# Performance work log

Measured on AMD Instinct MI355X. Metric: run time of the kernel, lower is better.

## Reference

```python
import jax, jax.numpy as jnp
import numpy as np

N = 1024          # nodes per atom and per input graph / barycenter
K = 8             # num_atoms
OT_LAYERS = 3     # proximal-point outer iterations inside fgwd
SINKHORN_LAYERS = 3
GWB_LAYERS = 2    # barycenter alternating-optimization iterations
PROX_BETA = 0.1   # proximal / entropic regularization strength
EPS = 1e-16


def fgwd(Gs, ps, Gb, pb):
    """Gromov-Wasserstein distance via proximal point + Sinkhorn.
    Gs:(ns,ns), ps:(ns,1), Gb:(nb,nb), pb:(nb,1). Returns (d, T) with T:(ns,nb).
    Square-loss GW cost: c(T) = f1(Gs) ps 1^T + 1 (f2(Gb) pb)^T - 2 Gs T Gb^T."""
    ns, nb = Gs.shape[0], Gb.shape[0]
    cost_st = ((Gs * Gs) @ ps) + ((Gb * Gb) @ pb).T  # (ns,1)+(1,nb) -> (ns,nb)
    T0 = ps @ pb.T  # independent-coupling init

    def ot_step(T, _):
        cost = cost_st - 2.0 * (Gs @ T @ Gb.T)
        kernel = jnp.exp(-cost / PROX_BETA) * T  # proximal-point kernel

        def sink(carry, _):
            a, b = carry
            b = pb / (kernel.T @ a + EPS)
            a = ps / (kernel @ b + EPS)
            return (a, b), None

        (a, b), _ = jax.lax.scan(sink, (ps, pb), None, length=SINKHORN_LAYERS)
        return (a * kernel) * b.T, None

    T, _ = jax.lax.scan(ot_step, T0, None, length=OT_LAYERS)
    cost = cost_st - 2.0 * (Gs @ T @ Gb.T)
    d = jnp.sum(cost * T)
    return d, T


def setup_inputs() -> dict:
    key = jax.random.key(0)
    k1, k2, k3 = jax.random.split(key, 3)
    Gm = jax.random.uniform(k1, (N, N), jnp.float32)          # input graph (sigmoid-range adjacency)
    pm = jnp.ones((N, 1), jnp.float32) / N                    # uniform node distribution
    atoms_presig = jax.random.normal(k2, (K, N, N), jnp.float32)  # pre-sigmoid atom params
    probs = jnp.ones((K, N, 1), jnp.float32) / N              # uniform atom distributions
    weights = jax.nn.softmax(jax.random.normal(k3, (K,), jnp.float32))  # output_weights
    return {"Gm": Gm, "pm": pm, "atoms_presig": atoms_presig, "probs": probs,
            "weights": weights}


def reference(Gm, pm, atoms_presig, probs, weights):
    Gk = jax.nn.sigmoid(atoms_presig)              # output_atoms: (K,N,N)
    G_bary, pb = Gm, pm                            # init_mode=0 -> barycenter init from input M
    fgwd_v = jax.vmap(fgwd, in_axes=(0, 0, None, None))
    denom = pb @ pb.T                              # pb pb^T normalizer
    for _ in range(GWB_LAYERS):
        _, trans = fgwd_v(Gk, probs, G_bary, pb)   # trans: (K,N,N)
        # comp_fgwb: sum_k w_k * T_k^T G_k T_k / (pb pb^T)
        GT = jnp.einsum('knm,kmj->knj', Gk, trans)
        G_bary = jnp.einsum('k,kni,knj->ij', weights, trans, GT) / denom
    d_fgw, _ = fgwd(Gm, pm, G_bary, pb)
    return d_fgw, G_bary
```

## Files before the change

kernel.cpp:

```cpp
#include <hip/hip_runtime.h>
#include <math.h>

#define N_   1024
#define K_   8
#define OTL  3
#define SKL  3
#define GWBL 2
#define INVB 10.0f
#define EPSV 1e-16f
#define INVN (1.0f / 1024.0f)
#define NN   ((size_t)N_ * N_)

typedef __attribute__((ext_vector_type(8))) short short8;
typedef __attribute__((ext_vector_type(4))) float f32x4;
typedef unsigned short bfu;

__device__ __forceinline__ float b2f(bfu u) {
    unsigned x = ((unsigned)u) << 16;
    return __builtin_bit_cast(float, x);
}
__device__ __forceinline__ bfu f2b(float f) {
    unsigned u = __builtin_bit_cast(unsigned, f);
    unsigned r = u + 0x7fffu + ((u >> 16) & 1u);
    return (bfu)(r >> 16);
}

template<int EPI>
__global__ __launch_bounds__(256, 2)
void bgemm_k(const bfu* __restrict__ A, const bfu* __restrict__ B,
             void* __restrict__ Cp, size_t sA, size_t sB, size_t sC,
             const float* __restrict__ rv, const float* __restrict__ cv,
             const float* __restrict__ wts, float* __restrict__ rs) {
    __shared__ bfu As[128 * 32];
    __shared__ bfu Bs[128 * 32];

    const int z  = blockIdx.x;
    const int bm = blockIdx.y * 128, bn = blockIdx.z * 128;
    const int tid = threadIdx.x;
    const int lane = tid & 63, wv = tid >> 6;
    const int wr = wv >> 1, wc = wv & 1;

    if (EPI == 0) {
        if (rs && blockIdx.y == 0 && blockIdx.z == 0) {
            float4 zf = {0.f, 0.f, 0.f, 0.f};
            *(float4*)&rs[z * N_ + tid * 4] = zf;
        }
    }

    const bfu* Az = A + (size_t)z * sA;
    const bfu* Bz = B + (size_t)z * sB;

    const int sr = tid >> 2;
    const int sk = (tid & 3) * 8;
    const int fr = lane & 15;
    const int ks = (lane >> 4) * 8;

    f32x4 acc[4][4];
    #pragma unroll
    for (int i = 0; i < 4; i++)
        #pragma unroll
        for (int j = 0; j < 4; j++) acc[i][j] = (f32x4)0.f;

    for (int k0 = 0; k0 < N_; k0 += 32) {
        __syncthreads();
        #pragma unroll
        for (int h = 0; h < 2; ++h) {
            const int row = sr + h * 64;
            const bfu* ga = Az + (size_t)(bm + row) * N_ + k0 + sk;
            const bfu* gb = Bz + (size_t)(bn + row) * N_ + k0 + sk;
            __builtin_amdgcn_global_load_lds(
                (const __attribute__((address_space(1))) unsigned int*)ga,
                (__attribute__((address_space(3))) unsigned int*)&As[row * 32 + sk],
                16, 0, 0);
            __builtin_amdgcn_global_load_lds(
                (const __attribute__((address_space(1))) unsigned int*)gb,
                (__attribute__((address_space(3))) unsigned int*)&Bs[row * 32 + sk],
                16, 0, 0);
        }
        __syncthreads();

        short8 af[4], bf[4];
        #pragma unroll
        for (int mi = 0; mi < 4; ++mi)
            af[mi] = *(const short8*)&As[(wr * 64 + mi * 16 + fr) * 32 + ks];
        #pragma unroll
        for (int ni = 0; ni < 4; ++ni)
            bf[ni] = *(const short8*)&Bs[(wc * 64 + ni * 16 + fr) * 32 + ks];
        #pragma unroll
        for (int mi = 0; mi < 4; ++mi)
            #pragma unroll
            for (int ni = 0; ni < 4; ++ni)
                acc[mi][ni] = __builtin_amdgcn_mfma_f32_16x16x32_bf16(
                    af[mi], bf[ni], acc[mi][ni], 0, 0, 0);
    }

    const int r0 = bm + wr * 64, c0 = bn + wc * 64;
    const int rq = (lane >> 4) * 4;

    if (EPI == 1) {
        float* Cz = (float*)Cp + (size_t)z * sC;
        const float w = wts[z];
        #pragma unroll
        for (int mi = 0; mi < 4; ++mi)
            #pragma unroll
            for (int ni = 0; ni < 4; ++ni)
                #pragma unroll
                for (int q = 0; q < 4; ++q)
                    Cz[(size_t)(r0 + mi * 16 + rq + q) * N_ + c0 + ni * 16 + fr]
                        = w * acc[mi][ni][q];
    } else if (EPI == 0) {
        bfu* Cz = (bfu*)Cp + (size_t)z * sC;
        #pragma unroll
        for (int mi = 0; mi < 4; ++mi)
            #pragma unroll
            for (int ni = 0; ni < 4; ++ni)
                #pragma unroll
                for (int q = 0; q < 4; ++q)
                    Cz[(size_t)(r0 + mi * 16 + rq + q) * N_ + c0 + ni * 16 + fr]
                        = f2b(acc[mi][ni][q]);
    } else {
        bfu* Cz = (bfu*)Cp + (size_t)z * sC;
        const float* rvz = rv + z * N_;
        float rsum[4][4];
        #pragma unroll
        for (int mi = 0; mi < 4; ++mi)
            #pragma unroll
            for (int q = 0; q < 4; ++q) rsum[mi][q] = 0.f;
        #pragma unroll
        for (int mi = 0; mi < 4; ++mi)
            #pragma unroll
            for (int ni = 0; ni < 4; ++ni)
                #pragma unroll
                for (int q = 0; q < 4; ++q) {
                    const int row = r0 + mi * 16 + rq + q;
                    const int col = c0 + ni * 16 + fr;
                    const float cost = rvz[col] + cv[row] - 2.f * acc[mi][ni][q];
                    const float t = b2f(Cz[(size_t)row * N_ + col]);
                    const bfu tn = f2b(expf(-cost * INVB) * t);
                    Cz[(size_t)row * N_ + col] = tn;
                    rsum[mi][q] += b2f(tn);
                }
        #pragma unroll
        for (int mi = 0; mi < 4; ++mi)
            #pragma unroll
            for (int q = 0; q < 4; ++q) {
                float v = rsum[mi][q];
                v += __shfl_xor(v, 1);
                v += __shfl_xor(v, 2);
                v += __shfl_xor(v, 4);
                v += __shfl_xor(v, 8);
                if (fr == 0)
                    atomicAdd(&rs[z * N_ + r0 + mi * 16 + rq + q], v);
            }
    }
}

__global__ __launch_bounds__(256, 2)
void gemm_splitk_k(const bfu* __restrict__ A, const bfu* __restrict__ B,
                   float* __restrict__ P) {
    __shared__ bfu As[128 * 32];
    __shared__ bfu Bs[128 * 32];
    const int bn = blockIdx.x * 128;
    const int bm = blockIdx.y * 128;
    const int kbase = blockIdx.z * 256;
    const int tid = threadIdx.x;
    const int lane = tid & 63, wv = tid >> 6;
    const int wr = wv >> 1, wc = wv & 1;
    const int sr = tid >> 2, sk = (tid & 3) * 8;
    const int fr = lane & 15, ks = (lane >> 4) * 8;

    f32x4 acc[4][4];
    #pragma unroll
    for (int i = 0; i < 4; i++)
        #pragma unroll
        for (int j = 0; j < 4; j++) acc[i][j] = (f32x4)0.f;

    for (int k0 = kbase; k0 < kbase + 256; k0 += 32) {
        __syncthreads();
        #pragma unroll
        for (int h = 0; h < 2; ++h) {
            const int row = sr + h * 64;
            __builtin_amdgcn_global_load_lds(
                (const __attribute__((address_space(1))) unsigned int*)
                    (A + (size_t)(bm + row) * N_ + k0 + sk),
                (__attribute__((address_space(3))) unsigned int*)&As[row * 32 + sk],
                16, 0, 0);
            __builtin_amdgcn_global_load_lds(
                (const __attribute__((address_space(1))) unsigned int*)
                    (B + (size_t)(bn + row) * N_ + k0 + sk),
                (__attribute__((address_space(3))) unsigned int*)&Bs[row * 32 + sk],
                16, 0, 0);
        }
        __syncthreads();
        short8 af[4], bf[4];
        #pragma unroll
        for (int mi = 0; mi < 4; ++mi)
            af[mi] = *(const short8*)&As[(wr * 64 + mi * 16 + fr) * 32 + ks];
        #pragma unroll
        for (int ni = 0; ni < 4; ++ni)
            bf[ni] = *(const short8*)&Bs[(wc * 64 + ni * 16 + fr) * 32 + ks];
        #pragma unroll
        for (int mi = 0; mi < 4; ++mi)
            #pragma unroll
            for (int ni = 0; ni < 4; ++ni)
                acc[mi][ni] = __builtin_amdgcn_mfma_f32_16x16x32_bf16(
                    af[mi], bf[ni], acc[mi][ni], 0, 0, 0);
    }

    float* Pz = P + (size_t)blockIdx.z * NN;
    const int r0 = bm + wr * 64, c0 = bn + wc * 64;
    const int rq = (lane >> 4) * 4;
    #pragma unroll
    for (int mi = 0; mi < 4; ++mi)
        #pragma unroll
        for (int ni = 0; ni < 4; ++ni)
            #pragma unroll
            for (int q = 0; q < 4; ++q)
                Pz[(size_t)(r0 + mi * 16 + rq + q) * N_ + c0 + ni * 16 + fr]
                    = acc[mi][ni][q];
}

template<int EPI>
__global__ void comb_k(const float* __restrict__ P, bfu* __restrict__ Tt,
                       const float* __restrict__ rv, const float* __restrict__ cv,
                       float* __restrict__ dout, const float* __restrict__ pb,
                       float* __restrict__ bv) {
    const int tid = threadIdx.x;
    if (EPI == 0) {
        if (dout && blockIdx.x == 0 && tid == 0) *dout = 0.f;
    }
    __shared__ float red[4];
    float bs = 0.f;
    #pragma unroll
    for (int rep = 0; rep < 2; ++rep) {
        const int row = blockIdx.x + rep * 512;
        const size_t idx = (size_t)row * N_ + tid * 4;
        float4 s = *(const float4*)(P + idx);
        #pragma unroll
        for (int sl = 1; sl < 4; ++sl) {
            float4 v = *(const float4*)(P + (size_t)sl * NN + idx);
            s.x += v.x; s.y += v.y; s.z += v.z; s.w += v.w;
        }
        if (EPI == 0) {
            bfu o[4];
            o[0] = f2b(s.x); o[1] = f2b(s.y); o[2] = f2b(s.z); o[3] = f2b(s.w);
            *(ulong1*)&Tt[idx] = *(ulong1*)o;
        } else {
            const int c = tid * 4;
            const float cvr = cv[row];
            const float4 rvc = *(const float4*)(rv + c);
            bfu t[4];
            *(ulong1*)t = *(const ulong1*)&Tt[idx];
            if (EPI == 2) {
                t[0] = f2b(expf(-(rvc.x + cvr - 2.f * s.x) * INVB) * b2f(t[0]));
                t[1] = f2b(expf(-(rvc.y + cvr - 2.f * s.y) * INVB) * b2f(t[1]));
                t[2] = f2b(expf(-(rvc.z + cvr - 2.f * s.z) * INVB) * b2f(t[2]));
                t[3] = f2b(expf(-(rvc.w + cvr - 2.f * s.w) * INVB) * b2f(t[3]));
                *(ulong1*)&Tt[idx] = *(ulong1*)t;
                float rsm = b2f(t[0]) + b2f(t[1]) + b2f(t[2]) + b2f(t[3]);
                #pragma unroll
                for (int off = 32; off; off >>= 1) rsm += __shfl_down(rsm, off);
                if ((tid & 63) == 0) red[tid >> 6] = rsm;
                __syncthreads();
                if (tid == 0)
                    bv[row] = pb[row] /
                        ((red[0] + red[1] + red[2] + red[3]) * INVN + EPSV);
                __syncthreads();
            } else {
                bs += (rvc.x + cvr - 2.f * s.x) * b2f(t[0]);
                bs += (rvc.y + cvr - 2.f * s.y) * b2f(t[1]);
                bs += (rvc.z + cvr - 2.f * s.z) * b2f(t[2]);
                bs += (rvc.w + cvr - 2.f * s.w) * b2f(t[3]);
            }
        }
    }
    if (EPI == 3) {
        #pragma unroll
        for (int off = 32; off; off >>= 1) bs += __shfl_down(bs, off);
        if ((tid & 63) == 0) red[tid >> 6] = bs;
        __syncthreads();
        if (tid == 0) atomicAdd(dout, red[0] + red[1] + red[2] + red[3]);
    }
}

__global__ __launch_bounds__(256)
void prox1_k(bfu* __restrict__ Tt, const float* __restrict__ c2,
             const float* __restrict__ u, const float* __restrict__ d2,
             const float* __restrict__ w, const float* __restrict__ ps,
             const float* __restrict__ pb, float* __restrict__ bv,
             int zs, int nb) {
    const int b = blockIdx.x;
    const int z  = (nb == 8) ? (b & 7) : 0;
    const int rp = (nb == 8) ? (b >> 3) : b;
    const int tid = threadIdx.x;
    const int half = tid >> 7;
    const int j = rp * 2 + half;
    const int i0 = (tid & 127) * 8;
    const float d2j = d2[j], wj = w[j], pbj = pb[j];
    const float* c2z = c2 + z * zs + i0;
    const float* uz  = u  + z * zs + i0;
    const float* psz = ps + z * zs + i0;
    bfu o[8];
    float s = 0.f;
    #pragma unroll
    for (int t = 0; t < 8; ++t) {
        const float cost = c2z[t] + d2j - 2.f * uz[t] * wj;
        o[t] = f2b(expf(-cost * INVB) * psz[t] * pbj);
        s += b2f(o[t]);
    }
    *(short8*)&Tt[((size_t)z << 20) + ((size_t)j << 10) + i0] = *(short8*)o;
    #pragma unroll
    for (int off = 32; off; off >>= 1) s += __shfl_down(s, off);
    __shared__ float red[4];
    if ((tid & 63) == 0) red[tid >> 6] = s;
    __syncthreads();
    if ((tid & 127) == 0)
        bv[z * N_ + j] = pbj / ((red[half * 2] + red[half * 2 + 1]) * INVN + EPSV);
}


__global__ void sinkb_k(const bfu* __restrict__ Tt, const float* __restrict__ a0,
                        const float* __restrict__ pb, float* __restrict__ bv) {
    int z, jb;
    if (gridDim.y == 8) { z = blockIdx.x & 7; jb = (blockIdx.x >> 3) + (blockIdx.y << 5); }
    else                { z = 0;              jb = blockIdx.x; }
    const int wv = threadIdx.x >> 6, lane = threadIdx.x & 63;
    const int j = jb * 4 + wv;
    const bfu* Tr = Tt + (size_t)z * NN + (size_t)j * N_;
    const float* az = a0 + z * N_;
    float s = 0.f;
    for (int c = lane * 8; c < N_; c += 512) {
        bfu t[8];
        *(short8*)t = *(const short8*)&Tr[c];
        #pragma unroll
        for (int q = 0; q < 8; ++q) s += b2f(t[q]) * az[c + q];
    }
    #pragma unroll
    for (int off = 32; off; off >>= 1) s += __shfl_down(s, off);
    if (lane == 0) bv[z * N_ + j] = pb[j] / (s + EPSV);
}

template<int NB, int RS, int TUPD>
__global__ __launch_bounds__(1024)
void sinka_k(bfu* __restrict__ Tt, const float* __restrict__ bvin,
             const float* __restrict__ rs, const float* __restrict__ ps, int pstr,
             float* __restrict__ av) {
    constexpr int CPB = (NB == 8) ? 32 : 16;
    constexpr int RG  = 1024 / CPB;
    constexpr int RPG = N_ / RG;
    int z, cb;
    if (NB == 8) { z = blockIdx.x & 7; cb = blockIdx.x >> 3; }
    else         { z = 0;              cb = blockIdx.x; }
    const int tid = threadIdx.x;
    const int cl = tid % CPB, rg = tid / CPB;
    const int i = cb * CPB + cl;
    bfu* Tz = Tt + (size_t)z * NN;

    __shared__ float bvs[1024];
    __shared__ float red[1024];
    if (RS) bvs[tid] = INVN / (rs[z * N_ + tid] * INVN + EPSV);
    else    bvs[tid] = bvin[z * N_ + tid];
    __syncthreads();

    float s = 0.f;
    const int j0 = rg * RPG;
    #pragma unroll 8
    for (int j = j0; j < j0 + RPG; ++j)
        s += b2f(Tz[(size_t)j * N_ + i]) * bvs[j];
    red[tid] = s;
    __syncthreads();
    #pragma unroll
    for (int h = RG / 2; h > 0; h >>= 1) {
        if (rg < h) red[rg * CPB + cl] += red[(rg + h) * CPB + cl];
        __syncthreads();
    }
    const float avi = ps[z * pstr + i] / (red[cl] + EPSV);
    if (!TUPD) {
        if (rg == 0) av[z * N_ + i] = avi;
    } else {
        for (int j = j0; j < j0 + RPG; ++j) {
            const size_t o = (size_t)j * N_ + i;
            Tz[o] = f2b(b2f(Tz[o]) * avi * bvs[j]);
        }
    }
}


template<int SIG>
__global__ void prep_k(const float* __restrict__ X, bfu* __restrict__ Y,
                       float* __restrict__ y2, float* __restrict__ y1) {
    const int z = blockIdx.y;
    const int wv = threadIdx.x >> 6, lane = threadIdx.x & 63;
    const int r = blockIdx.x * 4 + wv;
    const float* Xr = X + (size_t)z * NN + (size_t)r * N_;
    bfu* Yr = Y + (size_t)z * NN + (size_t)r * N_;
    float s2 = 0.f, s1 = 0.f;
    for (int c = lane * 4; c < N_; c += 256) {
        float4 v = *(const float4*)(Xr + c);
        if (SIG) {
            v.x = 1.f / (1.f + expf(-v.x));
            v.y = 1.f / (1.f + expf(-v.y));
            v.z = 1.f / (1.f + expf(-v.z));
            v.w = 1.f / (1.f + expf(-v.w));
        }
        bfu o[4];
        o[0] = f2b(v.x); o[1] = f2b(v.y); o[2] = f2b(v.z); o[3] = f2b(v.w);
        *(ulong1*)&Yr[c] = *(ulong1*)o;
        s2 += v.x * v.x + v.y * v.y + v.z * v.z + v.w * v.w;
        s1 += v.x + v.y + v.z + v.w;
    }
    #pragma unroll
    for (int off = 32; off; off >>= 1) {
        s2 += __shfl_down(s2, off);
        s1 += __shfl_down(s1, off);
    }
    if (lane == 0) {
        y2[z * N_ + r] = s2 * INVN;
        y1[z * N_ + r] = s1 * INVN;
    }
}

__global__ void reduce8_k(const float* __restrict__ part, bfu* __restrict__ Gbt,
                          float* __restrict__ d2, float* __restrict__ w,
                          float* __restrict__ out1) {
    const int tid = threadIdx.x;
    __shared__ float wred[2][8];
    #pragma unroll
    for (int rep = 0; rep < 2; ++rep) {
        const int row = blockIdx.x + rep * 512;
        const size_t idx = (size_t)row * N_ + tid * 4;
        float4 s = *(const float4*)(part + idx);
        #pragma unroll
        for (int sl = 1; sl < K_; ++sl) {
            float4 v = *(const float4*)(part + (size_t)sl * NN + idx);
            s.x += v.x; s.y += v.y; s.z += v.z; s.w += v.w;
        }
        const float sc = 1048576.f;
        s.x *= sc; s.y *= sc; s.z *= sc; s.w *= sc;
        bfu o[4];
        o[0] = f2b(s.x); o[1] = f2b(s.y); o[2] = f2b(s.z); o[3] = f2b(s.w);
        *(ulong1*)&Gbt[idx] = *(ulong1*)o;
        if (out1) {
            out1[idx + 0] = s.x; out1[idx + 1] = s.y;
            out1[idx + 2] = s.z; out1[idx + 3] = s.w;
        }
        float r2 = s.x * s.x + s.y * s.y + s.z * s.z + s.w * s.w;
        float r1 = s.x + s.y + s.z + s.w;
        #pragma unroll
        for (int off = 32; off; off >>= 1) {
            r2 += __shfl_down(r2, off);
            r1 += __shfl_down(r1, off);
        }
        if ((tid & 63) == 0) {
            wred[0][(tid >> 6) * 2]     = r2;
            wred[0][(tid >> 6) * 2 + 1] = r1;
        }
        __syncthreads();
        if (tid == 0) {
            d2[row] = (wred[0][0] + wred[0][2] + wred[0][4] + wred[0][6]) * INVN;
            w[row]  = (wred[0][1] + wred[0][3] + wred[0][5] + wred[0][7]) * INVN;
        }
        __syncthreads();
    }
}


template<int NB, int RS1>
static inline void sink_tail(bfu* Tt, const float* ps, int pstr, const float* pm,
                             float* avec, float* bvec, float* rs, hipStream_t stream) {
    const dim3 ga((NB == 8) ? 256 : 64);
    const dim3 gb(256, NB);
    const dim3 blk(256);
    sinka_k<NB, RS1, 0><<<ga, dim3(1024), 0, stream>>>(Tt, bvec, rs, ps, pstr, avec);
    sinkb_k<<<gb, blk, 0, stream>>>(Tt, avec, pm, bvec);
    sinka_k<NB, 0, 0><<<ga, dim3(1024), 0, stream>>>(Tt, bvec, rs, ps, pstr, avec);
    sinkb_k<<<gb, blk, 0, stream>>>(Tt, avec, pm, bvec);
    sinka_k<NB, 0, 1><<<ga, dim3(1024), 0, stream>>>(Tt, bvec, rs, ps, pstr, avec);
}

extern "C" void kernel_launch(void* const* d_in, const int* in_sizes, int n_in,
                              void* d_out, int out_size, void* d_ws, size_t ws_size,
                              hipStream_t stream) {
    const float* Gm    = (const float*)d_in[0];
    const float* pm    = (const float*)d_in[1];
    const float* atoms = (const float*)d_in[2];
    const float* probs = (const float*)d_in[3];
    const float* wts   = (const float*)d_in[4];
    float* out = (float*)d_out;

    char* base = (char*)d_ws;
    bfu*   Gkt  = (bfu*)base;                    base += K_ * NN * 2;
    bfu*   Tt   = (bfu*)base;                    base += K_ * NN * 2;
    bfu*   M    = (bfu*)base;                    base += K_ * NN * 2;
    float* part = (float*)base;                  base += K_ * NN * 4;
    bfu*   Gbt  = (bfu*)base;                    base += NN * 2;
    bfu*   Gmt  = (bfu*)base;                    base += NN * 2;
    float* Gk2ps = (float*)base;                 base += K_ * N_ * 4;
    float* Gku   = (float*)base;                 base += K_ * N_ * 4;
    float* Gm2pm = (float*)base;                 base += N_ * 4;
    float* Gmu   = (float*)base;                 base += N_ * 4;
    float* Gb2pb = (float*)base;                 base += N_ * 4;
    float* Gbw   = (float*)base;                 base += N_ * 4;
    float* avec  = (float*)base;                 base += K_ * N_ * 4;
    float* bvec  = (float*)base;                 base += K_ * N_ * 4;
    float* rs    = (float*)base;                 base += K_ * N_ * 4;

    const dim3 blk(256);
    const dim3 g8(8, 8, 8);
    const dim3 gsk(8, 8, 4);

    prep_k<1><<<dim3(256, K_), blk, 0, stream>>>(atoms, Gkt, Gk2ps, Gku);
    prep_k<0><<<dim3(256, 1), blk, 0, stream>>>(Gm, Gmt, Gm2pm, Gmu);

    for (int it = 0; it < GWBL; ++it) {
        const bfu*   GbtU = it ? Gbt : Gmt;
        const float* d2U  = it ? Gb2pb : Gm2pm;
        const float* wU   = it ? Gbw : Gmu;

        prox1_k<<<512 * K_, blk, 0, stream>>>(Tt, Gk2ps, Gku, d2U, wU,
                                              probs, pm, bvec, N_, K_);
        sink_tail<K_, 0>(Tt, probs, N_, pm, avec, bvec, rs, stream);
        for (int ot = 1; ot < OTL; ++ot) {
            bgemm_k<0><<<g8, blk, 0, stream>>>(Gkt, Tt, M, NN, NN, NN,
                nullptr, nullptr, nullptr, rs);
            bgemm_k<2><<<g8, blk, 0, stream>>>(GbtU, M, Tt, 0, NN, NN,
                Gk2ps, d2U, nullptr, rs);
            sink_tail<K_, 1>(Tt, probs, N_, pm, avec, bvec, rs, stream);
        }
        bgemm_k<0><<<g8, blk, 0, stream>>>(Tt, Gkt, M, NN, NN, NN,
            nullptr, nullptr, nullptr, nullptr);
        bgemm_k<1><<<g8, blk, 0, stream>>>(Tt, M, part, NN, NN, NN,
            nullptr, nullptr, wts, nullptr);
        reduce8_k<<<512, blk, 0, stream>>>(part, Gbt, Gb2pb, Gbw,
                                           (it == GWBL - 1) ? out + 1 : nullptr);
    }

    prox1_k<<<512, blk, 0, stream>>>(Tt, Gm2pm, Gmu, Gb2pb, Gbw, pm, pm, bvec, 0, 1);
    sink_tail<1, 0>(Tt, pm, 0, pm, avec, bvec, rs, stream);
    for (int ot = 1; ot < OTL; ++ot) {
        gemm_splitk_k<<<gsk, blk, 0, stream>>>(Gmt, Tt, part);
        comb_k<0><<<512, blk, 0, stream>>>(part, M, nullptr, nullptr,
                                           nullptr, nullptr, nullptr);
        gemm_splitk_k<<<gsk, blk, 0, stream>>>(Gbt, M, part);
        comb_k<2><<<512, blk, 0, stream>>>(part, Tt, Gm2pm, Gb2pb,
                                           nullptr, pm, bvec);
        sink_tail<1, 0>(Tt, pm, 0, pm, avec, bvec, rs, stream);
    }
    gemm_splitk_k<<<gsk, blk, 0, stream>>>(Gmt, Tt, part);
    comb_k<0><<<512, blk, 0, stream>>>(part, M, nullptr, nullptr,
                                       out , nullptr, nullptr);
    gemm_splitk_k<<<gsk, blk, 0, stream>>>(Gbt, M, part);
    comb_k<3><<<512, blk, 0, stream>>>(part, Tt, Gm2pm, Gb2pb, out, nullptr, nullptr);
}
```

Before: 684.3 us.

## Fuse Sinkhorn iterations into cooperative kernel and replace split-K GEMM with fused-epilogue tiles

The separate Sinkhorn row/column kernels become one cooperative kernel. It loops over all Sinkhorn iterations and uses grid-wide syncs in place of several kernel launches. The final single-graph GW stage now uses a 64x64-tile GEMM with the cost/exp, row-sum or distance epilogue fused in. This removes the split-K partial buffers and the separate combine kernels. The costs are grid.sync overhead, occupancy limits from requiring all 256 blocks of 1024 threads to be co-resident, and a smaller GEMM tile with less data reuse.

```diff
diff --git a/kernel.cpp b/kernel.cpp
--- a/kernel.cpp
+++ b/kernel.cpp
@@ -1,5 +1,8 @@
 #include <hip/hip_runtime.h>
+#include <hip/hip_cooperative_groups.h>
 #include <math.h>
+
+namespace cg = cooperative_groups;
 
 #define N_   1024
 #define K_   8
@@ -155,131 +158,132 @@
     }
 }
 
+template<int EPI>
 __global__ __launch_bounds__(256, 2)
-void gemm_splitk_k(const bfu* __restrict__ A, const bfu* __restrict__ B,
-                   float* __restrict__ P) {
-    __shared__ bfu As[128 * 32];
-    __shared__ bfu Bs[128 * 32];
-    const int bn = blockIdx.x * 128;
-    const int bm = blockIdx.y * 128;
-    const int kbase = blockIdx.z * 256;
+void gemm64_k(const bfu* __restrict__ A, const bfu* __restrict__ B,
+              void* __restrict__ Cp,
+              const float* __restrict__ rv, const float* __restrict__ cv,
+              float* __restrict__ rs, float* __restrict__ dout) {
+    __shared__ bfu As[64 * 32];
+    __shared__ bfu Bs[64 * 32];
+    const int bn = blockIdx.x * 64;
+    const int bm = blockIdx.y * 64;
     const int tid = threadIdx.x;
     const int lane = tid & 63, wv = tid >> 6;
     const int wr = wv >> 1, wc = wv & 1;
     const int sr = tid >> 2, sk = (tid & 3) * 8;
     const int fr = lane & 15, ks = (lane >> 4) * 8;
 
-    f32x4 acc[4][4];
+    if (EPI == 0) {
+        if (blockIdx.x == 0 && blockIdx.y == 0) {
+            if (rs) {
+                float4 zf = {0.f, 0.f, 0.f, 0.f};
+                *(float4*)&rs[tid * 4] = zf;
+            }
+            if (dout && tid == 0) *dout = 0.f;
+        }
+    }
+
+    f32x4 acc[2][2];
     #pragma unroll
-    for (int i = 0; i < 4; i++)
-        #pragma unroll
-        for (int j = 0; j < 4; j++) acc[i][j] = (f32x4)0.f;
-
-    for (int k0 = kbase; k0 < kbase + 256; k0 += 32) {
-        __syncthreads();
-        #pragma unroll
-        for (int h = 0; h < 2; ++h) {
-            const int row = sr + h * 64;
-            __builtin_amdgcn_global_load_lds(
-                (const __attribute__((address_space(1))) unsigned int*)
-                    (A + (size_t)(bm + row) * N_ + k0 + sk),
-                (__attribute__((address_space(3))) unsigned int*)&As[row * 32 + sk],
-                16, 0, 0);
-            __builtin_amdgcn_global_load_lds(
-                (const __attribute__((address_space(1))) unsigned int*)
-                    (B + (size_t)(bn + row) * N_ + k0 + sk),
-                (__attribute__((address_space(3))) unsigned int*)&Bs[row * 32 + sk],
-                16, 0, 0);
-        }
-        __syncthreads();
-        short8 af[4], bf[4];
-        #pragma unroll
-        for (int mi = 0; mi < 4; ++mi)
-            af[mi] = *(const short8*)&As[(wr * 64 + mi * 16 + fr) * 32 + ks];
-        #pragma unroll
-        for (int ni = 0; ni < 4; ++ni)
-            bf[ni] = *(const short8*)&Bs[(wc * 64 + ni * 16 + fr) * 32 + ks];
-        #pragma unroll
-        for (int mi = 0; mi < 4; ++mi)
-            #pragma unroll
-            for (int ni = 0; ni < 4; ++ni)
+    for (int i = 0; i < 2; i++)
+        #pragma unroll
+        for (int j = 0; j < 2; j++) acc[i][j] = (f32x4)0.f;
+
+    for (int k0 = 0; k0 < N_; k0 += 32) {
+        __syncthreads();
+        __builtin_amdgcn_global_load_lds(
+            (const __attribute__((address_space(1))) unsigned int*)
+                (A + (size_t)(bm + sr) * N_ + k0 + sk),
+            (__attribute__((address_space(3))) unsigned int*)&As[sr * 32 + sk],
+            16, 0, 0);
+        __builtin_amdgcn_global_load_lds(
+            (const __attribute__((address_space(1))) unsigned int*)
+                (B + (size_t)(bn + sr) * N_ + k0 + sk),
+            (__attribute__((address_space(3))) unsigned int*)&Bs[sr * 32 + sk],
+            16, 0, 0);
+        __syncthreads();
+        short8 af[2], bf[2];
+        #pragma unroll
+        for (int mi = 0; mi < 2; ++mi)
+            af[mi] = *(const short8*)&As[(wr * 32 + mi * 16 + fr) * 32 + ks];
+        #pragma unroll
+        for (int ni = 0; ni < 2; ++ni)
+            bf[ni] = *(const short8*)&Bs[(wc * 32 + ni * 16 + fr) * 32 + ks];
+        #pragma unroll
+        for (int mi = 0; mi < 2; ++mi)
+            #pragma unroll
+            for (int ni = 0; ni < 2; ++ni)
                 acc[mi][ni] = __builtin_amdgcn_mfma_f32_16x16x32_bf16(
                     af[mi], bf[ni], acc[mi][ni], 0, 0, 0);
     }
 
-    float* Pz = P + (size_t)blockIdx.z * NN;
-    const int r0 = bm + wr * 64, c0 = bn + wc * 64;
+    const int r0 = bm + wr * 32, c0 = bn + wc * 32;
     const int rq = (lane >> 4) * 4;
-    #pragma unroll
-    for (int mi = 0; mi < 4; ++mi)
-        #pragma unroll
-        for (int ni = 0; ni < 4; ++ni)
-            #pragma unroll
-            for (int q = 0; q < 4; ++q)
-                Pz[(size_t)(r0 + mi * 16 + rq + q) * N_ + c0 + ni * 16 + fr]
-                    = acc[mi][ni][q];
-}
-
-template<int EPI>
-__global__ void comb_k(const float* __restrict__ P, bfu* __restrict__ Tt,
-                       const float* __restrict__ rv, const float* __restrict__ cv,
-                       float* __restrict__ dout, const float* __restrict__ pb,
-                       float* __restrict__ bv) {
-    const int tid = threadIdx.x;
+
     if (EPI == 0) {
-        if (dout && blockIdx.x == 0 && tid == 0) *dout = 0.f;
-    }
-    __shared__ float red[4];
-    float bs = 0.f;
-    #pragma unroll
-    for (int rep = 0; rep < 2; ++rep) {
-        const int row = blockIdx.x + rep * 512;
-        const size_t idx = (size_t)row * N_ + tid * 4;
-        float4 s = *(const float4*)(P + idx);
-        #pragma unroll
-        for (int sl = 1; sl < 4; ++sl) {
-            float4 v = *(const float4*)(P + (size_t)sl * NN + idx);
-            s.x += v.x; s.y += v.y; s.z += v.z; s.w += v.w;
-        }
-        if (EPI == 0) {
-            bfu o[4];
-            o[0] = f2b(s.x); o[1] = f2b(s.y); o[2] = f2b(s.z); o[3] = f2b(s.w);
-            *(ulong1*)&Tt[idx] = *(ulong1*)o;
-        } else {
-            const int c = tid * 4;
-            const float cvr = cv[row];
-            const float4 rvc = *(const float4*)(rv + c);
-            bfu t[4];
-            *(ulong1*)t = *(const ulong1*)&Tt[idx];
-            if (EPI == 2) {
-                t[0] = f2b(expf(-(rvc.x + cvr - 2.f * s.x) * INVB) * b2f(t[0]));
-                t[1] = f2b(expf(-(rvc.y + cvr - 2.f * s.y) * INVB) * b2f(t[1]));
-                t[2] = f2b(expf(-(rvc.z + cvr - 2.f * s.z) * INVB) * b2f(t[2]));
-                t[3] = f2b(expf(-(rvc.w + cvr - 2.f * s.w) * INVB) * b2f(t[3]));
-                *(ulong1*)&Tt[idx] = *(ulong1*)t;
-                float rsm = b2f(t[0]) + b2f(t[1]) + b2f(t[2]) + b2f(t[3]);
-                #pragma unroll
-                for (int off = 32; off; off >>= 1) rsm += __shfl_down(rsm, off);
-                if ((tid & 63) == 0) red[tid >> 6] = rsm;
-                __syncthreads();
-                if (tid == 0)
-                    bv[row] = pb[row] /
-                        ((red[0] + red[1] + red[2] + red[3]) * INVN + EPSV);
-                __syncthreads();
-            } else {
-                bs += (rvc.x + cvr - 2.f * s.x) * b2f(t[0]);
-                bs += (rvc.y + cvr - 2.f * s.y) * b2f(t[1]);
-                bs += (rvc.z + cvr - 2.f * s.z) * b2f(t[2]);
-                bs += (rvc.w + cvr - 2.f * s.w) * b2f(t[3]);
+        bfu* C = (bfu*)Cp;
+        #pragma unroll
+        for (int mi = 0; mi < 2; ++mi)
+            #pragma unroll
+            for (int ni = 0; ni < 2; ++ni)
+                #pragma unroll
+                for (int q = 0; q < 4; ++q)
+                    C[(size_t)(r0 + mi * 16 + rq + q) * N_ + c0 + ni * 16 + fr]
+                        = f2b(acc[mi][ni][q]);
+    } else if (EPI == 2) {
+        bfu* C = (bfu*)Cp;
+        float rsum[2][4];
+        #pragma unroll
+        for (int mi = 0; mi < 2; ++mi)
+            #pragma unroll
+            for (int q = 0; q < 4; ++q) rsum[mi][q] = 0.f;
+        #pragma unroll
+        for (int mi = 0; mi < 2; ++mi)
+            #pragma unroll
+            for (int ni = 0; ni < 2; ++ni)
+                #pragma unroll
+                for (int q = 0; q < 4; ++q) {
+                    const int row = r0 + mi * 16 + rq + q;
+                    const int col = c0 + ni * 16 + fr;
+                    const float cost = rv[col] + cv[row] - 2.f * acc[mi][ni][q];
+                    const float t = b2f(C[(size_t)row * N_ + col]);
+                    const bfu tn = f2b(expf(-cost * INVB) * t);
+                    C[(size_t)row * N_ + col] = tn;
+                    rsum[mi][q] += b2f(tn);
+                }
+        #pragma unroll
+        for (int mi = 0; mi < 2; ++mi)
+            #pragma unroll
+            for (int q = 0; q < 4; ++q) {
+                float v = rsum[mi][q];
+                v += __shfl_xor(v, 1);
+                v += __shfl_xor(v, 2);
+                v += __shfl_xor(v, 4);
+                v += __shfl_xor(v, 8);
+                if (fr == 0)
+                    atomicAdd(&rs[r0 + mi * 16 + rq + q], v);
             }
-        }
-    }
-    if (EPI == 3) {
+    } else {
+        const bfu* C = (const bfu*)Cp;
+        float bs = 0.f;
+        #pragma unroll
+        for (int mi = 0; mi < 2; ++mi)
+            #pragma unroll
+            for (int ni = 0; ni < 2; ++ni)
+                #pragma unroll
+                for (int q = 0; q < 4; ++q) {
+                    const int row = r0 + mi * 16 + rq + q;
+                    const int col = c0 + ni * 16 + fr;
+                    bs += (rv[col] + cv[row] - 2.f * acc[mi][ni][q]) *
+                          b2f(C[(size_t)row * N_ + col]);
+                }
         #pragma unroll
         for (int off = 32; off; off >>= 1) bs += __shfl_down(bs, off);
-        if ((tid & 63) == 0) red[tid >> 6] = bs;
-        __syncthreads();
-        if (tid == 0) atomicAdd(dout, red[0] + red[1] + red[2] + red[3]);
+        __shared__ float wred[4];
+        if (lane == 0) wred[wv] = bs;
+        __syncthreads();
+        if (tid == 0) atomicAdd(dout, wred[0] + wred[1] + wred[2] + wred[3]);
     }
 }
 
@@ -318,69 +322,79 @@
         bv[z * N_ + j] = pbj / ((red[half * 2] + red[half * 2 + 1]) * INVN + EPSV);
 }
 
-
-__global__ void sinkb_k(const bfu* __restrict__ Tt, const float* __restrict__ a0,
-                        const float* __restrict__ pb, float* __restrict__ bv) {
-    int z, jb;
-    if (gridDim.y == 8) { z = blockIdx.x & 7; jb = (blockIdx.x >> 3) + (blockIdx.y << 5); }
-    else                { z = 0;              jb = blockIdx.x; }
-    const int wv = threadIdx.x >> 6, lane = threadIdx.x & 63;
-    const int j = jb * 4 + wv;
-    const bfu* Tr = Tt + (size_t)z * NN + (size_t)j * N_;
-    const float* az = a0 + z * N_;
-    float s = 0.f;
-    for (int c = lane * 8; c < N_; c += 512) {
-        bfu t[8];
-        *(short8*)t = *(const short8*)&Tr[c];
-        #pragma unroll
-        for (int q = 0; q < 8; ++q) s += b2f(t[q]) * az[c + q];
-    }
-    #pragma unroll
-    for (int off = 32; off; off >>= 1) s += __shfl_down(s, off);
-    if (lane == 0) bv[z * N_ + j] = pb[j] / (s + EPSV);
-}
-
-template<int NB, int RS, int TUPD>
-__global__ __launch_bounds__(1024)
-void sinka_k(bfu* __restrict__ Tt, const float* __restrict__ bvin,
-             const float* __restrict__ rs, const float* __restrict__ ps, int pstr,
-             float* __restrict__ av) {
+template<int NB, int RS1>
+__global__ __launch_bounds__(1024, 1)
+void sink_fused_k(bfu* __restrict__ Tt, const float* __restrict__ rs,
+                  const float* __restrict__ bv1,
+                  const float* __restrict__ ps, int pstr,
+                  const float* __restrict__ pb,
+                  float* __restrict__ av, float* __restrict__ bv) {
+    cg::grid_group grid = cg::this_grid();
     constexpr int CPB = (NB == 8) ? 32 : 16;
     constexpr int RG  = 1024 / CPB;
     constexpr int RPG = N_ / RG;
+    constexpr int RPB = (NB == 8) ? 32 : 16;
+    constexpr int RPW = RPB / 16;
+
+    const int blk = blockIdx.x;
     int z, cb;
-    if (NB == 8) { z = blockIdx.x & 7; cb = blockIdx.x >> 3; }
-    else         { z = 0;              cb = blockIdx.x; }
+    if (NB == 8) { z = blk & 7; cb = blk >> 3; }
+    else         { z = 0;       cb = blk; }
     const int tid = threadIdx.x;
     const int cl = tid % CPB, rg = tid / CPB;
     const int i = cb * CPB + cl;
+    const int wv = tid >> 6, lane = tid & 63;
+    const int rb0 = cb * RPB;
+    const int zN = z * N_;
     bfu* Tz = Tt + (size_t)z * NN;
+    const float psv = ps[z * pstr + i];
+    const int j0 = rg * RPG;
 
     __shared__ float bvs[1024];
     __shared__ float red[1024];
-    if (RS) bvs[tid] = INVN / (rs[z * N_ + tid] * INVN + EPSV);
-    else    bvs[tid] = bvin[z * N_ + tid];
-    __syncthreads();
-
-    float s = 0.f;
-    const int j0 = rg * RPG;
-    #pragma unroll 8
-    for (int j = j0; j < j0 + RPG; ++j)
-        s += b2f(Tz[(size_t)j * N_ + i]) * bvs[j];
-    red[tid] = s;
-    __syncthreads();
-    #pragma unroll
-    for (int h = RG / 2; h > 0; h >>= 1) {
-        if (rg < h) red[rg * CPB + cl] += red[(rg + h) * CPB + cl];
-        __syncthreads();
-    }
-    const float avi = ps[z * pstr + i] / (red[cl] + EPSV);
-    if (!TUPD) {
-        if (rg == 0) av[z * N_ + i] = avi;
-    } else {
-        for (int j = j0; j < j0 + RPG; ++j) {
-            const size_t o = (size_t)j * N_ + i;
-            Tz[o] = f2b(b2f(Tz[o]) * avi * bvs[j]);
+
+    for (int it = 0; it < SKL; ++it) {
+        if (it == 0) bvs[tid] = RS1 ? (INVN / (rs[zN + tid] * INVN + EPSV))
+                                    : bv1[zN + tid];
+        else         bvs[tid] = bv[zN + tid];
+        __syncthreads();
+        float s = 0.f;
+        #pragma unroll 8
+        for (int j = j0; j < j0 + RPG; ++j)
+            s += b2f(Tz[(size_t)j * N_ + i]) * bvs[j];
+        red[tid] = s;
+        __syncthreads();
+        #pragma unroll
+        for (int h = RG / 2; h > 0; h >>= 1) {
+            if (rg < h) red[rg * CPB + cl] += red[(rg + h) * CPB + cl];
+            __syncthreads();
+        }
+        const float avi = psv / (red[cl] + EPSV);
+        if (it == SKL - 1) {
+            for (int j = j0; j < j0 + RPG; ++j) {
+                const size_t o = (size_t)j * N_ + i;
+                Tz[o] = f2b(b2f(Tz[o]) * avi * bvs[j]);
+            }
+        } else {
+            if (rg == 0) av[zN + i] = avi;
+            grid.sync();
+            #pragma unroll
+            for (int rr = 0; rr < RPW; ++rr) {
+                const int j = rb0 + wv * RPW + rr;
+                const bfu* Tr = Tz + (size_t)j * N_;
+                const float* az = av + zN;
+                float sb = 0.f;
+                for (int c = lane * 8; c < N_; c += 512) {
+                    bfu t[8];
+                    *(short8*)t = *(const short8*)&Tr[c];
+                    #pragma unroll
+                    for (int q = 0; q < 8; ++q) sb += b2f(t[q]) * az[c + q];
+                }
+                #pragma unroll
+                for (int off = 32; off; off >>= 1) sb += __shfl_down(sb, off);
+                if (lane == 0) bv[zN + j] = pb[j] / (sb + EPSV);
+            }
+            grid.sync();
         }
     }
 }
@@ -424,7 +438,7 @@
                           float* __restrict__ d2, float* __restrict__ w,
                           float* __restrict__ out1) {
     const int tid = threadIdx.x;
-    __shared__ float wred[2][8];
+    __shared__ float wred[8];
     #pragma unroll
     for (int rep = 0; rep < 2; ++rep) {
         const int row = blockIdx.x + rep * 512;
@@ -452,31 +466,18 @@
             r1 += __shfl_down(r1, off);
         }
         if ((tid & 63) == 0) {
-            wred[0][(tid >> 6) * 2]     = r2;
-            wred[0][(tid >> 6) * 2 + 1] = r1;
+            wred[(tid >> 6) * 2]     = r2;
+            wred[(tid >> 6) * 2 + 1] = r1;
         }
         __syncthreads();
         if (tid == 0) {
-            d2[row] = (wred[0][0] + wred[0][2] + wred[0][4] + wred[0][6]) * INVN;
-            w[row]  = (wred[0][1] + wred[0][3] + wred[0][5] + wred[0][7]) * INVN;
-        }
-        __syncthreads();
-    }
-}
-
-
-template<int NB, int RS1>
-static inline void sink_tail(bfu* Tt, const float* ps, int pstr, const float* pm,
-                             float* avec, float* bvec, float* rs, hipStream_t stream) {
-    const dim3 ga((NB == 8) ? 256 : 64);
-    const dim3 gb(256, NB);
-    const dim3 blk(256);
-    sinka_k<NB, RS1, 0><<<ga, dim3(1024), 0, stream>>>(Tt, bvec, rs, ps, pstr, avec);
-    sinkb_k<<<gb, blk, 0, stream>>>(Tt, avec, pm, bvec);
-    sinka_k<NB, 0, 0><<<ga, dim3(1024), 0, stream>>>(Tt, bvec, rs, ps, pstr, avec);
-    sinkb_k<<<gb, blk, 0, stream>>>(Tt, avec, pm, bvec);
-    sinka_k<NB, 0, 1><<<ga, dim3(1024), 0, stream>>>(Tt, bvec, rs, ps, pstr, avec);
-}
+            d2[row] = (wred[0] + wred[2] + wred[4] + wred[6]) * INVN;
+            w[row]  = (wred[1] + wred[3] + wred[5] + wred[7]) * INVN;
+        }
+        __syncthreads();
+    }
+}
+
 
 extern "C" void kernel_launch(void* const* d_in, const int* in_sizes, int n_in,
                               void* d_out, int out_size, void* d_ws, size_t ws_size,
@@ -507,7 +508,17 @@
 
     const dim3 blk(256);
     const dim3 g8(8, 8, 8);
-    const dim3 gsk(8, 8, 4);
+    const dim3 g64(16, 16);
+
+    bfu* TtP = Tt;
+    float* rsP = rs;
+    float* bvecP = bvec;
+    const float* probsP = probs;
+    const float* pmP = pm;
+    float* avP = avec;
+    int pstrN = N_, pstr0 = 0;
+    void* argsB[] = { &TtP, &rsP, &bvecP, &probsP, &pstrN, &pmP, &avP, &bvecP };
+    void* args1[] = { &TtP, &rsP, &bvecP, &pmP,    &pstr0, &pmP, &avP, &bvecP };
 
     prep_k<1><<<dim3(256, K_), blk, 0, stream>>>(atoms, Gkt, Gk2ps, Gku);
     prep_k<0><<<dim3(256, 1), blk, 0, stream>>>(Gm, Gmt, Gm2pm, Gmu);
@@ -519,13 +530,15 @@
 
         prox1_k<<<512 * K_, blk, 0, stream>>>(Tt, Gk2ps, Gku, d2U, wU,
                                               probs, pm, bvec, N_, K_);
-        sink_tail<K_, 0>(Tt, probs, N_, pm, avec, bvec, rs, stream);
+        hipLaunchCooperativeKernel((const void*)sink_fused_k<K_, 0>,
+            dim3(256), dim3(1024), argsB, 0, stream);
         for (int ot = 1; ot < OTL; ++ot) {
             bgemm_k<0><<<g8, blk, 0, stream>>>(Gkt, Tt, M, NN, NN, NN,
                 nullptr, nullptr, nullptr, rs);
             bgemm_k<2><<<g8, blk, 0, stream>>>(GbtU, M, Tt, 0, NN, NN,
                 Gk2ps, d2U, nullptr, rs);
-            sink_tail<K_, 1>(Tt, probs, N_, pm, avec, bvec, rs, stream);
+            hipLaunchCooperativeKernel((const void*)sink_fused_k<K_, 1>,
+                dim3(256), dim3(1024), argsB, 0, stream);
         }
         bgemm_k<0><<<g8, blk, 0, stream>>>(Tt, Gkt, M, NN, NN, NN,
             nullptr, nullptr, nullptr, nullptr);
@@ -536,19 +549,18 @@
     }
 
     prox1_k<<<512, blk, 0, stream>>>(Tt, Gm2pm, Gmu, Gb2pb, Gbw, pm, pm, bvec, 0, 1);
-    sink_tail<1, 0>(Tt, pm, 0, pm, avec, bvec, rs, stream);
+    hipLaunchCooperativeKernel((const void*)sink_fused_k<1, 0>,
+        dim3(64), dim3(1024), args1, 0, stream);
     for (int ot = 1; ot < OTL; ++ot) {
-        gemm_splitk_k<<<gsk, blk, 0, stream>>>(Gmt, Tt, part);
-        comb_k<0><<<512, blk, 0, stream>>>(part, M, nullptr, nullptr,
-                                           nullptr, nullptr, nullptr);
-        gemm_splitk_k<<<gsk, blk, 0, stream>>>(Gbt, M, part);
-        comb_k<2><<<512, blk, 0, stream>>>(part, Tt, Gm2pm, Gb2pb,
-                                           nullptr, pm, bvec);
-        sink_tail<1, 0>(Tt, pm, 0, pm, avec, bvec, rs, stream);
-    }
-    gemm_splitk_k<<<gsk, blk, 0, stream>>>(Gmt, Tt, part);
-    comb_k<0><<<512, blk, 0, stream>>>(part, M, nullptr, nullptr,
-                                       out , nullptr, nullptr);
-    gemm_splitk_k<<<gsk, blk, 0, stream>>>(Gbt, M, part);
-    comb_k<3><<<512, blk, 0, stream>>>(part, Tt, Gm2pm, Gb2pb, out, nullptr, nullptr);
-}
+        gemm64_k<0><<<g64, blk, 0, stream>>>(Gmt, Tt, M,
+            nullptr, nullptr, rs, nullptr);
+        gemm64_k<2><<<g64, blk, 0, stream>>>(Gbt, M, Tt,
+            Gm2pm, Gb2pb, rs, nullptr);
+        hipLaunchCooperativeKernel((const void*)sink_fused_k<1, 1>,
+            dim3(64), dim3(1024), args1, 0, stream);
+    }
+    gemm64_k<0><<<g64, blk, 0, stream>>>(Gmt, Tt, M,
+        nullptr, nullptr, nullptr, out );
+    gemm64_k<3><<<g64, blk, 0, stream>>>(Gbt, M, Tt,
+        Gm2pm, Gb2pb, nullptr, out);
+}
```

Result: slower. 1.500 ms (+119.2%).
